# Performance work log

Hardware: AMD Instinct MI355X
Metric: run time of the kernel (lower is better)

## Reference

```python
import jax, jax.numpy as jnp
import numpy as np

B, T, C, NH = 8, 1024, 1024, 16
DH = C // NH  # 64


def setup_inputs() -> dict:
    key = jax.random.key(0)
    ks = jax.random.split(key, 7)
    s = 1.0 / np.sqrt(C)
    return {
        "x": jax.random.normal(ks[0], (B, T, C), dtype=jnp.float32),
        "Wq": jax.random.normal(ks[1], (C, C), dtype=jnp.float32) * s,
        "bq": jnp.zeros((C,), dtype=jnp.float32),
        "Wk": jax.random.normal(ks[2], (C, C), dtype=jnp.float32) * s,
        "bk": jnp.zeros((C,), dtype=jnp.float32),
        "Wv": jax.random.normal(ks[3], (C, C), dtype=jnp.float32) * s,
        "bv": jnp.zeros((C,), dtype=jnp.float32),
    }


def reference(x, Wq, bq, Wk, bk, Wv, bv):
    # Linear projections (weights stored as [in, out])
    q = x @ Wq + bq  # [B, T, C]
    k = x @ Wk + bk
    v = x @ Wv + bv
    q = q.reshape(B, T, NH, DH)
    k = k.reshape(B, T, NH, DH)
    v = v.reshape(B, T, NH, DH)
    scale = 1.0 / np.sqrt(DH)
    # NOTE: source module's causal mask buffer is all-ones due to a non-inplace
    # masked_fill bug, so attention is NON-causal (mask multiply is a no-op).
    attn = jnp.einsum("bqhd,bkhd->bhqk", q, k) * scale  # [B, NH, T, T]
    attn = jax.nn.softmax(attn, axis=-1)
    # dropout is identity (p=0 / eval)
    o = jnp.einsum("bhqk,bkhd->bqhd", attn, v)  # [B, T, NH, DH]
    return o.reshape(B, T, C)
```

## Files before the change

### kernel.cpp

```cpp
#include <hip/hip_runtime.h>


#define B_  8
#define T_  1024
#define C_  1024
#define NH_ 16
#define DH_ 64
#define M_  (B_ * T_)

typedef __bf16 bf16x8 __attribute__((ext_vector_type(8)));
typedef float  floatx4 __attribute__((ext_vector_type(4)));
typedef float  floatx16 __attribute__((ext_vector_type(16)));
typedef unsigned int uintx4 __attribute__((ext_vector_type(4)));

__device__ __forceinline__ unsigned short f2bf(float f) {
    unsigned int u = __float_as_uint(f);
    unsigned int r = (u + 0x7fffu + ((u >> 16) & 1u)) >> 16;
    return (unsigned short)r;
}

__device__ __forceinline__ unsigned int f2bf2(float a, float b) {
    unsigned int ua = __float_as_uint(a), ub = __float_as_uint(b);
    ua += 0x7fffu + ((ua >> 16) & 1u);
    ub += 0x7fffu + ((ub >> 16) & 1u);
#if __has_builtin(__builtin_amdgcn_perm)
    return __builtin_amdgcn_perm(ub, ua, 0x07060302u);
#else
    return (ua >> 16) | (ub & 0xffff0000u);
#endif
}

__device__ __forceinline__ float fexp2(float x) {
#if __has_builtin(__builtin_amdgcn_exp2f)
    return __builtin_amdgcn_exp2f(x);
#else
    return exp2f(x);
#endif
}

__device__ __forceinline__ void gload_lds16(const void* g, void* l) {
    __builtin_amdgcn_global_load_lds(
        (const __attribute__((address_space(1))) unsigned int*)g,
        (__attribute__((address_space(3))) unsigned int*)l, 16, 0, 0);
}

__global__ __launch_bounds__(256) void prep_kernel(
    const float* __restrict__ x, unsigned short* __restrict__ xb,
    const float* __restrict__ Wq, const float* __restrict__ Wk,
    const float* __restrict__ Wv, unsigned short* __restrict__ WtAll)
{
    int blk = blockIdx.x;
    if (blk < 8192) {
        int i = blk * 256 + threadIdx.x;
        float4 v = ((const float4*)x)[i];
        ushort4 o;
        unsigned int lo = f2bf2(v.x, v.y), hi = f2bf2(v.z, v.w);
        o.x = (unsigned short)lo; o.y = (unsigned short)(lo >> 16);
        o.z = (unsigned short)hi; o.w = (unsigned short)(hi >> 16);
        ((ushort4*)xb)[i] = o;
        return;
    }
    int tb3 = blk - 8192;
    int which = tb3 >> 8;
    int tb = tb3 & 255;
    const float* W = (which == 0) ? Wq : ((which == 1) ? Wk : Wv);
    unsigned short* out = WtAll + (size_t)which * C_ * C_;

    __shared__ __align__(16) unsigned short tile[64 * 68];
    int k0 = (tb >> 4) * 64, n0 = (tb & 15) * 64;
    int c = threadIdx.x & 63, r0 = threadIdx.x >> 6;

    for (int j = 0; j < 16; ++j) {
        int r = r0 + j * 4;
        tile[c * 68 + r] = f2bf(W[(size_t)(k0 + r) * C_ + n0 + c]);
    }
    __syncthreads();
    int k4 = (threadIdx.x & 15) * 4;
    int nw = threadIdx.x >> 4;
    for (int it = 0; it < 4; ++it) {
        int n = nw + it * 16;
        ushort4 o = *(const ushort4*)&tile[n * 68 + k4];
        *(ushort4*)&out[(size_t)(n0 + n) * C_ + k0 + k4] = o;
    }
}

__global__ __launch_bounds__(256) void qkv_gemm_kernel(
    const unsigned short* __restrict__ xb,
    const unsigned short* __restrict__ WtAll,
    const float* __restrict__ bq, const float* __restrict__ bk,
    const float* __restrict__ bv,
    unsigned short* __restrict__ Qb, unsigned short* __restrict__ Kb,
    unsigned short* __restrict__ Vt)
{
    int which = blockIdx.z;
    const unsigned short* W = WtAll + (size_t)which * C_ * C_;
    const float* bias = (which == 0) ? bq : ((which == 1) ? bk : bv);
    float oscale = (which == 0) ? 0.125f * 1.44269504f : 1.0f;

    __shared__ __align__(16) unsigned short As[128 * 64];
    __shared__ __align__(16) unsigned short Bs[128 * 64];

    int tid = threadIdx.x;
    int wave = tid >> 6, lane = tid & 63;
    int quad = lane >> 4, l16 = lane & 15, l7 = l16 & 7;
    int wm = wave >> 1, wn = wave & 1;
    int bm = blockIdx.x, bn = blockIdx.y;

    floatx4 acc[4][4] = {};

    for (int kk = 0; kk < C_; kk += 64) {
        __syncthreads();
        #pragma unroll
        for (int i = 0; i < 4; ++i) {
            int c = (wave * 4 + i) * 64 + lane;
            int row = c >> 3;
            int lcol = ((c & 7) ^ (row & 7)) * 8;
            gload_lds16(&xb[(size_t)(bm * 128 + row) * C_ + kk + lcol],
                        &As[(wave * 4 + i) * 512]);
            gload_lds16(&W[(size_t)(bn * 128 + row) * C_ + kk + lcol],
                        &Bs[(wave * 4 + i) * 512]);
        }
        __syncthreads();
        #pragma unroll
        for (int s = 0; s < 2; ++s) {
            bf16x8 a[4], bfr[4];
            #pragma unroll
            for (int mt = 0; mt < 4; ++mt) {
                int row = wm * 64 + mt * 16 + l16;
                a[mt] = *(const bf16x8*)&As[row * 64 + ((s * 4 + quad) ^ l7) * 8];
            }
            #pragma unroll
            for (int nt = 0; nt < 4; ++nt) {
                int row = wn * 64 + nt * 16 + l16;
                bfr[nt] = *(const bf16x8*)&Bs[row * 64 + ((s * 4 + quad) ^ l7) * 8];
            }
            if (which < 2) {
                #pragma unroll
                for (int mt = 0; mt < 4; ++mt)
                    #pragma unroll
                    for (int nt = 0; nt < 4; ++nt)
                        acc[mt][nt] = __builtin_amdgcn_mfma_f32_16x16x32_bf16(
                            bfr[nt], a[mt], acc[mt][nt], 0, 0, 0);
            } else {
                #pragma unroll
                for (int mt = 0; mt < 4; ++mt)
                    #pragma unroll
                    for (int nt = 0; nt < 4; ++nt)
                        acc[mt][nt] = __builtin_amdgcn_mfma_f32_16x16x32_bf16(
                            a[mt], bfr[nt], acc[mt][nt], 0, 0, 0);
            }
        }
    }

    if (which < 2) {
        unsigned short* outp = (which == 0) ? Qb : Kb;
        #pragma unroll
        for (int mt = 0; mt < 4; ++mt) {
            int tg = bm * 128 + wm * 64 + mt * 16 + l16;
            int bb = tg >> 10, t = tg & (T_ - 1);
            #pragma unroll
            for (int nt = 0; nt < 4; ++nt) {
                int colg = bn * 128 + wn * 64 + nt * 16 + quad * 4;
                int h = colg >> 6, d = colg & 63;
                float4 b4 = *(const float4*)&bias[colg];
                uint2 o;
                o.x = f2bf2((acc[mt][nt][0] + b4.x) * oscale,
                            (acc[mt][nt][1] + b4.y) * oscale);
                o.y = f2bf2((acc[mt][nt][2] + b4.z) * oscale,
                            (acc[mt][nt][3] + b4.w) * oscale);
                *(uint2*)&outp[((size_t)(bb * NH_ + h) * T_ + t) * DH_ + d] = o;
            }
        }
    } else {
        int quadp = ((quad & 1) << 1) | (quad >> 1);
        #pragma unroll
        for (int nt = 0; nt < 4; ++nt) {
            int colg = bn * 128 + wn * 64 + nt * 16 + l16;
            int h = colg >> 6, d = colg & 63;
            float bval = bias[colg];
            #pragma unroll
            for (int mt = 0; mt < 4; ++mt) {
                int tg = bm * 128 + wm * 64 + mt * 16 + quadp * 4;
                int bb = tg >> 10, t = tg & (T_ - 1);
                uint2 o;
                o.x = f2bf2(acc[mt][nt][0] + bval, acc[mt][nt][1] + bval);
                o.y = f2bf2(acc[mt][nt][2] + bval, acc[mt][nt][3] + bval);
                *(uint2*)&Vt[((size_t)(bb * NH_ + h) * DH_ + d) * T_ + t] = o;
            }
        }
    }
}

__global__ __launch_bounds__(256) void attn_kernel(
    const unsigned short* __restrict__ Qb,
    const unsigned short* __restrict__ Kb,
    const unsigned short* __restrict__ Vt,
    float* __restrict__ out)
{
    int bh = blockIdx.x;
    int qblk = blockIdx.y;
    int b = bh >> 4, h = bh & (NH_ - 1);
    int tid = threadIdx.x;
    int wave = tid >> 6, lane = tid & 63;
    int l5 = lane & 31, hi = lane >> 5;

    const unsigned short* Qh = Qb + (size_t)bh * T_ * DH_;
    const unsigned short* Kh = Kb + (size_t)bh * T_ * DH_;
    const unsigned short* Vh = Vt + (size_t)bh * DH_ * T_;

    __shared__ __align__(16) unsigned short Ks[2][128 * 64];
    __shared__ __align__(16) unsigned short Vs[2][64 * 128];

    int qrow = qblk * 128 + wave * 32 + l5;
    bf16x8 qa[4];
    #pragma unroll
    for (int sl = 0; sl < 4; ++sl)
        qa[sl] = *(const bf16x8*)&Qh[(size_t)qrow * DH_ + sl * 16 + hi * 8];

    uintx4 ou; ou.x = ou.y = ou.z = ou.w = 0x3F803F80u;
    bf16x8 ones = __builtin_bit_cast(bf16x8, ou);

    floatx16 o_acc[2] = {};
    floatx16 o_sum = {};

    auto stage = [&](int kt2, int bb) {
        #pragma unroll
        for (int i = 0; i < 4; ++i) {
            int c = (wave * 4 + i) * 64 + lane;
            int krow = c >> 3;
            int klcol = ((c & 7) ^ (krow & 7)) * 8;
            gload_lds16(&Kh[(size_t)(kt2 * 128 + krow) * DH_ + klcol],
                        &Ks[bb][(wave * 4 + i) * 512]);
            int vrow = c >> 4;
            int vlcol = ((c & 15) ^ (vrow & 15)) * 8;
            gload_lds16(&Vh[(size_t)vrow * T_ + kt2 * 128 + vlcol],
                        &Vs[bb][(wave * 4 + i) * 512]);
        }
    };

    stage(0, 0);
    for (int kt2 = 0; kt2 < T_ / 128; ++kt2) {
        int cur = kt2 & 1;
        __syncthreads();
        if (kt2 + 1 < T_ / 128) stage(kt2 + 1, cur ^ 1);

        #pragma unroll
        for (int kh = 0; kh < 2; ++kh) {
            #pragma unroll
            for (int nt = 0; nt < 2; ++nt) {
                floatx16 st = {};
                int r = kh * 64 + nt * 32 + l5;
                #pragma unroll
                for (int sl = 0; sl < 4; ++sl) {
                    bf16x8 kb = *(const bf16x8*)&Ks[cur][r * 64 + ((sl * 2 + hi) ^ (r & 7)) * 8];
                    st = __builtin_amdgcn_mfma_f32_32x32x16_bf16(kb, qa[sl], st, 0, 0, 0);
                }

                unsigned int pd[8];
                #pragma unroll
                for (int m = 0; m < 8; ++m) {
                    float e0 = fexp2(st[2 * m]);
                    float e1 = fexp2(st[2 * m + 1]);
                    pd[m] = f2bf2(e0, e1);
                }

                #pragma unroll
                for (int ks2 = 0; ks2 < 2; ++ks2) {
                    uintx4 pbu;
                    pbu.x = pd[ks2 * 4 + 0];
                    pbu.y = pd[ks2 * 4 + 1];
                    pbu.z = pd[ks2 * 4 + 2];
                    pbu.w = pd[ks2 * 4 + 3];
                    bf16x8 pb = __builtin_bit_cast(bf16x8, pbu);
                    o_sum = __builtin_amdgcn_mfma_f32_32x32x16_bf16(
                        ones, pb, o_sum, 0, 0, 0);
                    int ch = kh * 8 + nt * 4 + ks2 * 2 + hi;
                    #pragma unroll
                    for (int dt = 0; dt < 2; ++dt) {
                        int vr = dt * 32 + l5;
                        bf16x8 vb = *(const bf16x8*)&Vs[cur][vr * 128 + (ch ^ (vr & 15)) * 8];
                        o_acc[dt] = __builtin_amdgcn_mfma_f32_32x32x16_bf16(
                            vb, pb, o_acc[dt], 0, 0, 0);
                    }
                }
            }
        }
    }

    float inv = 1.0f / o_sum[0];
    int t = qblk * 128 + wave * 32 + l5;
    float* op = &out[((size_t)b * T_ + t) * C_ + h * DH_];
    #pragma unroll
    for (int dt = 0; dt < 2; ++dt) {
        #pragma unroll
        for (int g = 0; g < 4; ++g) {
            float4 v;
            v.x = o_acc[dt][g * 4 + 0] * inv;
            v.y = o_acc[dt][g * 4 + 1] * inv;
            v.z = o_acc[dt][g * 4 + 2] * inv;
            v.w = o_acc[dt][g * 4 + 3] * inv;
            *(float4*)&op[dt * 32 + g * 8 + hi * 4] = v;
        }
    }
}

extern "C" void kernel_launch(void* const* d_in, const int* in_sizes, int n_in,
                              void* d_out, int out_size, void* d_ws, size_t ws_size,
                              hipStream_t stream) {
    const float* x  = (const float*)d_in[0];
    const float* Wq = (const float*)d_in[1];
    const float* bq = (const float*)d_in[2];
    const float* Wk = (const float*)d_in[3];
    const float* bk = (const float*)d_in[4];
    const float* Wv = (const float*)d_in[5];
    const float* bv = (const float*)d_in[6];
    float* out = (float*)d_out;

    char* ws = (char*)d_ws;
    size_t off = 0;
    unsigned short* xb = (unsigned short*)(ws + off); off += (size_t)M_ * C_ * 2;
    unsigned short* Wt = (unsigned short*)(ws + off); off += (size_t)3 * C_ * C_ * 2;
    unsigned short* Qb = (unsigned short*)(ws + off); off += (size_t)M_ * C_ * 2;
    unsigned short* Kb = (unsigned short*)(ws + off); off += (size_t)M_ * C_ * 2;
    unsigned short* Vt = (unsigned short*)(ws + off); off += (size_t)M_ * C_ * 2;

    prep_kernel<<<dim3(8960), dim3(256), 0, stream>>>(x, xb, Wq, Wk, Wv, Wt);

    qkv_gemm_kernel<<<dim3(M_ / 128, C_ / 128, 3), dim3(256), 0, stream>>>(
        xb, Wt, bq, bk, bv, Qb, Kb, Vt);

    attn_kernel<<<dim3(B_ * NH_, T_ / 128), dim3(256), 0, stream>>>(Qb, Kb, Vt, out);
}
```

Measured before the change: 217.8 us.

## Double-buffer QKV GEMM LDS tiles with async prefetch two stages ahead

Converts the QKV projection GEMM main loop to a double-buffered LDS pipeline. Tile k+2 is loaded directly into LDS while the MFMAs for tile k run, using explicit vmcnt/lgkmcnt waits and barriers in place of two __syncthreads per iteration. It also adds a min-blocks-per-CU hint of 2 to launch_bounds. The cost is doubled LDS use, 64KB per block, which may limit occupancy, and hand-tuned waitcnt values that must match the number of outstanding loads.

```diff
diff --git a/kernel.cpp b/kernel.cpp
--- a/kernel.cpp
+++ b/kernel.cpp
@@ -84,7 +84,7 @@
     }
 }
 
-__global__ __launch_bounds__(256) void qkv_gemm_kernel(
+__global__ __launch_bounds__(256, 2) void qkv_gemm_kernel(
     const unsigned short* __restrict__ xb,
     const unsigned short* __restrict__ WtAll,
     const float* __restrict__ bq, const float* __restrict__ bk,
@@ -97,8 +97,8 @@
     const float* bias = (which == 0) ? bq : ((which == 1) ? bk : bv);
     float oscale = (which == 0) ? 0.125f * 1.44269504f : 1.0f;
 
-    __shared__ __align__(16) unsigned short As[128 * 64];
-    __shared__ __align__(16) unsigned short Bs[128 * 64];
+    __shared__ __align__(16) unsigned short As[2][128 * 64];
+    __shared__ __align__(16) unsigned short Bs[2][128 * 64];
 
     int tid = threadIdx.x;
     int wave = tid >> 6, lane = tid & 63;
@@ -108,48 +108,70 @@
 
     floatx4 acc[4][4] = {};
 
-    for (int kk = 0; kk < C_; kk += 64) {
-        __syncthreads();
+    auto stage = [&](int kt, int bb) {
         #pragma unroll
         for (int i = 0; i < 4; ++i) {
             int c = (wave * 4 + i) * 64 + lane;
             int row = c >> 3;
             int lcol = ((c & 7) ^ (row & 7)) * 8;
-            gload_lds16(&xb[(size_t)(bm * 128 + row) * C_ + kk + lcol],
-                        &As[(wave * 4 + i) * 512]);
-            gload_lds16(&W[(size_t)(bn * 128 + row) * C_ + kk + lcol],
-                        &Bs[(wave * 4 + i) * 512]);
-        }
-        __syncthreads();
+            gload_lds16(&xb[(size_t)(bm * 128 + row) * C_ + kt * 64 + lcol],
+                        &As[bb][(wave * 4 + i) * 512]);
+            gload_lds16(&W[(size_t)(bn * 128 + row) * C_ + kt * 64 + lcol],
+                        &Bs[bb][(wave * 4 + i) * 512]);
+        }
+    };
+
+    stage(0, 0);
+    stage(1, 1);
+    asm volatile("s_waitcnt vmcnt(8)" ::: "memory");
+    __builtin_amdgcn_s_barrier();
+    __builtin_amdgcn_sched_barrier(0);
+
+    for (int kt = 0; kt < 16; ++kt) {
+        int cur = kt & 1;
+        bf16x8 a[2][4], bfr[2][4];
         #pragma unroll
         for (int s = 0; s < 2; ++s) {
-            bf16x8 a[4], bfr[4];
             #pragma unroll
             for (int mt = 0; mt < 4; ++mt) {
                 int row = wm * 64 + mt * 16 + l16;
-                a[mt] = *(const bf16x8*)&As[row * 64 + ((s * 4 + quad) ^ l7) * 8];
+                a[s][mt] = *(const bf16x8*)&As[cur][row * 64 + ((s * 4 + quad) ^ l7) * 8];
             }
             #pragma unroll
             for (int nt = 0; nt < 4; ++nt) {
                 int row = wn * 64 + nt * 16 + l16;
-                bfr[nt] = *(const bf16x8*)&Bs[row * 64 + ((s * 4 + quad) ^ l7) * 8];
-            }
+                bfr[s][nt] = *(const bf16x8*)&Bs[cur][row * 64 + ((s * 4 + quad) ^ l7) * 8];
+            }
+        }
+        asm volatile("s_waitcnt lgkmcnt(0)" ::: "memory");
+        __builtin_amdgcn_s_barrier();
+        __builtin_amdgcn_sched_barrier(0);
+
+        if (kt + 2 < 16) stage(kt + 2, cur);
+
+        #pragma unroll
+        for (int s = 0; s < 2; ++s) {
             if (which < 2) {
                 #pragma unroll
                 for (int mt = 0; mt < 4; ++mt)
                     #pragma unroll
                     for (int nt = 0; nt < 4; ++nt)
                         acc[mt][nt] = __builtin_amdgcn_mfma_f32_16x16x32_bf16(
-                            bfr[nt], a[mt], acc[mt][nt], 0, 0, 0);
+                            bfr[s][nt], a[s][mt], acc[mt][nt], 0, 0, 0);
             } else {
                 #pragma unroll
                 for (int mt = 0; mt < 4; ++mt)
                     #pragma unroll
                     for (int nt = 0; nt < 4; ++nt)
                         acc[mt][nt] = __builtin_amdgcn_mfma_f32_16x16x32_bf16(
-                            a[mt], bfr[nt], acc[mt][nt], 0, 0, 0);
-            }
-        }
+                            a[s][mt], bfr[s][nt], acc[mt][nt], 0, 0, 0);
+            }
+        }
+
+        if (kt < 14) asm volatile("s_waitcnt vmcnt(8)" ::: "memory");
+        else         asm volatile("s_waitcnt vmcnt(0)" ::: "memory");
+        __builtin_amdgcn_s_barrier();
+        __builtin_amdgcn_sched_barrier(0);
     }
 
     if (which < 2) {
```

Measured after the change: 219.0 us. About the same (+0.6%).
